# Kernel tuning notes

Measured on AMD Instinct MI355X. Metric: run time of the kernel, lower is better.

Reference implementation:

```python
import jax, jax.numpy as jnp
import numpy as np

N_NODES = 30000
N_EDGES = 480000
C_IN = 256
D_HEAD = 64   # out_channels
N_HEADS = 4
M_FEAT = 30   # nb_random_features
K_GUMBEL = 10
TAU = 0.25


def _linear_init(key, out_f, in_f):
    s = 1.0 / np.sqrt(in_f)
    k1, k2 = jax.random.split(key)
    w = jax.random.uniform(k1, (out_f, in_f), minval=-s, maxval=s, dtype=jnp.float32)
    b = jax.random.uniform(k2, (out_f,), minval=-s, maxval=s, dtype=jnp.float32)
    return w, b


def setup_inputs() -> dict:
    key = jax.random.key(0)
    ks = jax.random.split(key, 8)
    z = jax.random.normal(ks[0], (1, N_NODES, C_IN), dtype=jnp.float32)
    edge_index = jax.random.randint(ks[1], (2, N_EDGES), 0, N_NODES)
    # Gumbel(0,1)/tau noise, matching torch's (-Exp(1).log())/tau
    u = jax.random.uniform(ks[2], (N_NODES, 1, N_HEADS, K_GUMBEL), dtype=jnp.float32,
                           minval=1e-8, maxval=1.0)
    gumbels = -jnp.log(-jnp.log(u)) / TAU
    # Performer orthogonal random-feature projection matrix [M, D]
    rng = np.random.default_rng(0)
    q, _ = np.linalg.qr(rng.standard_normal((D_HEAD, D_HEAD)))
    q = q.T[:M_FEAT]
    mult = np.linalg.norm(rng.standard_normal((M_FEAT, D_HEAD)), axis=1)
    proj = jnp.asarray(np.diag(mult) @ q, dtype=jnp.float32)
    Wq_w, Wq_b = _linear_init(ks[3], N_HEADS * D_HEAD, C_IN)
    Wk_w, Wk_b = _linear_init(ks[4], N_HEADS * D_HEAD, C_IN)
    Wv_w, Wv_b = _linear_init(ks[5], N_HEADS * D_HEAD, C_IN)
    Wo_w, Wo_b = _linear_init(ks[6], D_HEAD, N_HEADS * D_HEAD)
    b = jnp.full((1, N_HEADS), 0.1, dtype=jnp.float32)  # rb_order=1, sigmoid init
    tau = jnp.float32(TAU)
    return {"z": z, "edge_index": edge_index, "tau": tau, "gumbels": gumbels,
            "proj": proj, "Wq_w": Wq_w, "Wq_b": Wq_b, "Wk_w": Wk_w, "Wk_b": Wk_b,
            "Wv_w": Wv_w, "Wv_b": Wv_b, "Wo_w": Wo_w, "Wo_b": Wo_b, "b": b}


def _softmax_kernel_feats(data, proj, is_query):
    # data: [B, N, H, D] -> phi(data): [B, N, H, M]
    dn = 1.0 / jnp.sqrt(jnp.sqrt(jnp.float32(data.shape[-1])))
    data = data * dn
    ratio = 1.0 / jnp.sqrt(jnp.float32(proj.shape[0]))
    dash = jnp.einsum('bnhd,md->bnhm', data, proj)
    diag = jnp.sum(data * data, axis=-1, keepdims=True) * 0.5
    if is_query:
        stab = jnp.max(dash, axis=-1, keepdims=True)
    else:
        stab = jnp.max(dash, axis=(1, 3), keepdims=True)
    return ratio * (jnp.exp(dash - diag - stab) + 1e-6)


def reference(z, edge_index, tau, gumbels, proj, Wq_w, Wq_b, Wk_w, Wk_b,
              Wv_w, Wv_b, Wo_w, Wo_b, b):
    B, N, _ = z.shape
    M, D = proj.shape
    H = Wq_w.shape[0] // D
    query = (z @ Wq_w.T + Wq_b).reshape(B, N, H, D)
    key = (z @ Wk_w.T + Wk_b).reshape(B, N, H, D)
    value = (z @ Wv_w.T + Wv_b).reshape(B, N, H, D)

    inv_sqrt_tau = 1.0 / jnp.sqrt(tau)
    qp = jnp.transpose(_softmax_kernel_feats(query * inv_sqrt_tau, proj, True), (1, 0, 2, 3))   # [N,B,H,M]
    kp = jnp.transpose(_softmax_kernel_feats(key * inv_sqrt_tau, proj, False), (1, 0, 2, 3))    # [N,B,H,M]
    v = jnp.transpose(value, (1, 0, 2, 3))                                                       # [N,B,H,D]

    # Gumbel-perturbed key features: [N,B,H,K,M]
    kg = kp[:, :, :, None, :] * jnp.exp(gumbels)[..., None]
    kvs = jnp.einsum('nbhkm,nbhd->bhkmd', kg, v)
    z_num = jnp.einsum('nbhm,bhkmd->nbhkd', qp, kvs)      # [N,B,H,K,D]
    z_den = jnp.einsum('nbhm,bhkm->nbhk', qp, kg.sum(axis=0))
    z_out = jnp.transpose(jnp.mean(z_num / z_den[..., None], axis=3), (1, 0, 2, 3))  # [B,N,H,D]

    # edge attention weights (for link loss)
    start, end = edge_index[0], edge_index[1]
    edge_num = jnp.transpose(jnp.einsum('ebhm,ebhm->ebh', qp[end], kp[start]), (1, 0, 2))  # [B,E,H]
    attn_norm = jnp.einsum('nbhm,bhm->nbh', qp, kp.sum(axis=0))
    edge_dem = jnp.transpose(attn_norm[end], (1, 0, 2))
    A_weight = edge_num / edge_dem

    # relational bias (rb_order=1, sigmoid), degree-normalized sparse conv over value
    ones_e = jnp.ones(start.shape[0], dtype=jnp.float32)
    d_in = jax.ops.segment_sum(ones_e, end, num_segments=N)
    d_out = jax.ops.segment_sum(ones_e, start, num_segments=N)
    edge_w = jax.nn.sigmoid(b[0])[None, :] * jnp.sqrt((1.0 / d_in[end]) * (1.0 / d_out[start]))[:, None]  # [E,H]
    conv = jax.vmap(lambda vb: jax.ops.segment_sum(vb[start] * edge_w[:, :, None], end,
                                                   num_segments=N))(value)
    z_out = z_out + conv

    z_next = z_out.reshape(B, N, H * D) @ Wo_w.T + Wo_b  # [B,N,D]

    d_norm = 1.0 / d_in[end]
    link_loss = jnp.mean(jnp.log(A_weight) * d_norm[None, :, None])
    return z_next, link_loss
```

## Files before the change

### kernel.cpp

```cpp
#include <hip/hip_runtime.h>
#include <hip/hip_bf16.h>

#define NN 30000
#define NE 480000
#define NH 4
#define DH 64
#define MF 30
#define KG 10
#define RATIO 0.18257418583505536f
#define DNRM  0.35355339059327373f

#define P_WF    0
#define P_BF    196608
#define P_WOF   197376
#define P_WOBF  213760
#define P_BBF   213824
#define P_PROJ  213828
#define P_TAU   215748
#define P_TOTAL 215749

typedef unsigned short u16;
typedef unsigned int   u32;
typedef __attribute__((ext_vector_type(8))) short bf16x8;
typedef __attribute__((ext_vector_type(4))) float f32x4;

__device__ __forceinline__ float u2f(u16 u) { return __uint_as_float(((u32)u) << 16); }
__device__ __forceinline__ u16  f2bf(float f) {
    u32 x = __float_as_uint(f);
    return (u16)((x + 0x7FFFu + ((x >> 16) & 1u)) >> 16);
}
__device__ __forceinline__ u32  encf(float f) { u32 u = __float_as_uint(f); return (u & 0x80000000u) ? ~u : (u | 0x80000000u); }
__device__ __forceinline__ float decf(u32 u)  { return (u & 0x80000000u) ? __uint_as_float(u & 0x7FFFFFFFu) : __uint_as_float(~u); }

__global__ void k_detect(const u16* __restrict__ z, int* __restrict__ flag) {
    if (threadIdx.x == 0 && blockIdx.x == 0) {
        int bad = 0;
        for (int i = 0; i < 256; i += 2) {
            u16 u = z[i];
            int e = (u >> 7) & 0xFF;
            if (u != 0 && !(e >= 100 && e <= 140)) bad++;
        }
        *flag = (bad > 16) ? 1 : 0;
    }
}

__global__ __launch_bounds__(256) void k_cvt_params(
    const void* Wq, const void* Wk, const void* Wv,
    const void* bq, const void* bk, const void* bv,
    const void* Wo, const void* Wob, const void* bb, const void* proj,
    const void* taup, float* __restrict__ params, const int* __restrict__ flag)
{
    int i = blockIdx.x * 256 + threadIdx.x;
    if (i >= P_TOTAL) return;
    int f = *flag;
    if (i == P_TAU) {
        float v = f ? ((const float*)taup)[0] : u2f(((const u16*)taup)[0]);
        if (!(v > 1e-6f && v < 1e6f)) {
            float ff = ((const float*)taup)[0];
            v = (ff > 1e-6f && ff < 1e6f) ? ff : 0.25f;
        }
        params[i] = v;
        return;
    }
    const void* src; int j;
    if      (i < 65536)  { src = Wq;  j = i; }
    else if (i < 131072) { src = Wk;  j = i - 65536; }
    else if (i < 196608) { src = Wv;  j = i - 131072; }
    else if (i < 196864) { src = bq;  j = i - 196608; }
    else if (i < 197120) { src = bk;  j = i - 196864; }
    else if (i < 197376) { src = bv;  j = i - 197120; }
    else if (i < 213760) { src = Wo;  j = i - 197376; }
    else if (i < 213824) { src = Wob; j = i - 213760; }
    else if (i < 213828) { src = bb;  j = i - 213824; }
    else                 { src = proj; j = i - P_PROJ; }
    params[i] = f ? ((const float*)src)[j] : u2f(((const u16*)src)[j]);
}

__global__ __launch_bounds__(256) void k_cvt_w(const float* __restrict__ params,
                                               u16* __restrict__ Wh, u16* __restrict__ Wl)
{
    int i = blockIdx.x * 256 + threadIdx.x;
    float x = params[P_WF + i];
    u16 h = f2bf(x);
    Wh[i] = h;
    Wl[i] = f2bf(x - u2f(h));
}

__global__ __launch_bounds__(256) void k_deg(const int* __restrict__ ei, int* __restrict__ din, int* __restrict__ dout) {
    int e = blockIdx.x * 256 + threadIdx.x;
    if (e >= NE) return;
    atomicAdd(&dout[ei[e]], 1);
    atomicAdd(&din[ei[NE + e]], 1);
}

__global__ __launch_bounds__(256) void k_off(const int* __restrict__ din, int* __restrict__ offn, int* __restrict__ counter) {
    __shared__ int s[256];
    __shared__ int base;
    int tid = threadIdx.x;
    int n = blockIdx.x * 256 + tid;
    int v = (n < NN) ? din[n] : 0;
    s[tid] = v;
    __syncthreads();
    for (int o = 1; o < 256; o <<= 1) {
        int t = (tid >= o) ? s[tid - o] : 0;
        __syncthreads();
        s[tid] += t;
        __syncthreads();
    }
    if (tid == 255) base = atomicAdd(counter, s[255]);
    __syncthreads();
    if (n < NN) offn[n] = base + s[tid] - v;
}

__global__ __launch_bounds__(256) void k_fill(const int* __restrict__ ei, const int* __restrict__ offn,
                                              int* __restrict__ fill, int* __restrict__ csr,
                                              const int* __restrict__ din, const int* __restrict__ dout,
                                              float* __restrict__ wedge) {
    int e = blockIdx.x * 256 + threadIdx.x;
    if (e >= NE) return;
    int s = ei[e], t = ei[NE + e];
    int pos = offn[t] + atomicAdd(&fill[t], 1);
    csr[pos] = s;
    wedge[pos] = rsqrtf((float)din[t] * (float)dout[s]);
}

__global__ __launch_bounds__(256) void k_gemm_feat(
    const void* __restrict__ zv, const float* __restrict__ params, const int* __restrict__ flag,
    const u16* __restrict__ Wh, const u16* __restrict__ Wl,
    u16* __restrict__ V16, float* __restrict__ qp, u16* __restrict__ qp16,
    float* __restrict__ dashK, float* __restrict__ diagK, u32* __restrict__ stab)
{
    __shared__ __align__(16) char smemc[32768];
    __shared__ u32 smaxL;
    char* AsH = smemc;
    char* AsL = smemc + 8192;
    char* BsH = smemc + 16384;
    char* BsL = smemc + 24576;
    float* tile  = (float*)smemc;
    float* projL = (float*)smemc + 4352;

    const int tid = threadIdx.x;
    const int bm = blockIdx.x * 64;
    const int bn = blockIdx.y * 64;
    const int f32 = *flag;
    const int wave = tid >> 6, lane = tid & 63;
    const int wm = wave >> 1, wn = wave & 1;
    const int sr = tid >> 2;
    const int sc = (tid & 3) * 16;

    f32x4 acc[2][2] = {};

    for (int k0 = 0; k0 < 256; k0 += 64) {
        __syncthreads();
        {
            int zrow = bm + sr;
            if (f32) {
                float x[16];
                if (zrow < NN) {
                    const float4* zp = (const float4*)((const float*)zv + (size_t)zrow * 256 + k0 + sc);
                    #pragma unroll
                    for (int q4 = 0; q4 < 4; ++q4) {
                        float4 v = zp[q4];
                        x[q4 * 4 + 0] = v.x; x[q4 * 4 + 1] = v.y;
                        x[q4 * 4 + 2] = v.z; x[q4 * 4 + 3] = v.w;
                    }
                } else {
                    #pragma unroll
                    for (int j = 0; j < 16; ++j) x[j] = 0.f;
                }
                #pragma unroll
                for (int j8 = 0; j8 < 2; ++j8) {
                    u32 hw[4], lw[4];
                    #pragma unroll
                    for (int p = 0; p < 4; ++p) {
                        float a = x[j8 * 8 + 2 * p], b2 = x[j8 * 8 + 2 * p + 1];
                        u16 ha = f2bf(a), hb = f2bf(b2);
                        hw[p] = (u32)ha | ((u32)hb << 16);
                        u16 la = f2bf(a - u2f(ha)), lb = f2bf(b2 - u2f(hb));
                        lw[p] = (u32)la | ((u32)lb << 16);
                    }
                    int byt = sr * 128 + (((sc + j8 * 8) * 2) ^ ((sr & 7) << 4));
                    *(uint4*)(AsH + byt) = make_uint4(hw[0], hw[1], hw[2], hw[3]);
                    *(uint4*)(AsL + byt) = make_uint4(lw[0], lw[1], lw[2], lw[3]);
                }
            } else {
                uint4 v0 = make_uint4(0, 0, 0, 0), v1 = v0;
                if (zrow < NN) {
                    const uint4* zp = (const uint4*)((const u16*)zv + (size_t)zrow * 256 + k0 + sc);
                    v0 = zp[0]; v1 = zp[1];
                }
                int byt0 = sr * 128 + (((sc + 0) * 2) ^ ((sr & 7) << 4));
                int byt1 = sr * 128 + (((sc + 8) * 2) ^ ((sr & 7) << 4));
                *(uint4*)(AsH + byt0) = v0;
                *(uint4*)(AsH + byt1) = v1;
            }
        }
        {
            int byt0 = sr * 128 + (((sc + 0) * 2) ^ ((sr & 7) << 4));
            int byt1 = sr * 128 + (((sc + 8) * 2) ^ ((sr & 7) << 4));
            const uint4* wh4 = (const uint4*)(Wh + (size_t)(bn + sr) * 256 + k0 + sc);
            *(uint4*)(BsH + byt0) = wh4[0];
            *(uint4*)(BsH + byt1) = wh4[1];
            if (f32) {
                const uint4* wl4 = (const uint4*)(Wl + (size_t)(bn + sr) * 256 + k0 + sc);
                *(uint4*)(BsL + byt0) = wl4[0];
                *(uint4*)(BsL + byt1) = wl4[1];
            }
        }
        __syncthreads();
        #pragma unroll
        for (int kk = 0; kk < 2; ++kk) {
            const int kb = (kk * 32 + ((lane >> 4) * 8)) * 2;
            bf16x8 ah[2], bh[2], al[2], bl[2];
            #pragma unroll
            for (int i = 0; i < 2; ++i) {
                int ar = 32 * wm + 16 * i + (lane & 15);
                int ab = ar * 128 + (kb ^ ((ar & 7) << 4));
                ah[i] = *(const bf16x8*)(AsH + ab);
                int br = 32 * wn + 16 * i + (lane & 15);
                int bb2 = br * 128 + (kb ^ ((br & 7) << 4));
                bh[i] = *(const bf16x8*)(BsH + bb2);
                if (f32) {
                    al[i] = *(const bf16x8*)(AsL + ab);
                    bl[i] = *(const bf16x8*)(BsL + bb2);
                }
            }
            #pragma unroll
            for (int i = 0; i < 2; ++i)
                #pragma unroll
                for (int nf = 0; nf < 2; ++nf) {
                    acc[i][nf] = __builtin_amdgcn_mfma_f32_16x16x32_bf16(ah[i], bh[nf], acc[i][nf], 0, 0, 0);
                    if (f32) {
                        acc[i][nf] = __builtin_amdgcn_mfma_f32_16x16x32_bf16(ah[i], bl[nf], acc[i][nf], 0, 0, 0);
                        acc[i][nf] = __builtin_amdgcn_mfma_f32_16x16x32_bf16(al[i], bh[nf], acc[i][nf], 0, 0, 0);
                    }
                }
        }
    }
    __syncthreads();

    const float* bfv = params + P_BF;
    if (bn >= 512) {
        #pragma unroll
        for (int i = 0; i < 2; ++i)
            #pragma unroll
            for (int nf = 0; nf < 2; ++nf) {
                int col = 32 * wn + 16 * nf + (lane & 15);
                float bias = bfv[bn + col];
                #pragma unroll
                for (int r2 = 0; r2 < 4; ++r2) {
                    int row = 32 * wm + 16 * i + ((lane >> 4) * 4) + r2;
                    tile[row * 68 + col] = acc[i][nf][r2] + bias;
                }
            }
        __syncthreads();
        for (int i2 = tid; i2 < 4096; i2 += 256) {
            int row = i2 >> 6, col = i2 & 63;
            int nrow = bm + row;
            if (nrow < NN) V16[(size_t)nrow * 256 + (bn - 512) + col] = f2bf(tile[row * 68 + col]);
        }
        return;
    }

    for (int i2 = tid; i2 < MF * DH; i2 += 256) projL[(i2 >> 6) * 65 + (i2 & 63)] = params[P_PROJ + i2];
    if (tid == 0) smaxL = 0u;
    float scale = DNRM * rsqrtf(params[P_TAU]);
    #pragma unroll
    for (int i = 0; i < 2; ++i)
        #pragma unroll
        for (int nf = 0; nf < 2; ++nf) {
            int col = 32 * wn + 16 * nf + (lane & 15);
            float bias = bfv[bn + col];
            #pragma unroll
            for (int r2 = 0; r2 < 4; ++r2) {
                int row = 32 * wm + 16 * i + ((lane >> 4) * 4) + r2;
                tile[row * 68 + col] = (acc[i][nf][r2] + bias) * scale;
            }
        }
    __syncthreads();

    int r = tid >> 2, q = tid & 3;
    int n = bm + r;
    const float* trow = tile + r * 68;
    float dp = 0.f;
    #pragma unroll
    for (int d = q * 16; d < q * 16 + 16; ++d) dp += trow[d] * trow[d];
    dp += __shfl_xor(dp, 1);
    dp += __shfl_xor(dp, 2);
    float diag = dp * 0.5f;

    float dm[8];
    int nm = 0;
    float lmax = -3.0e38f;
    for (int m = q; m < MF; m += 4) {
        float s = 0.f;
        #pragma unroll
        for (int d = 0; d < DH; ++d) s += trow[d] * projL[m * 65 + d];
        dm[nm++] = s;
        lmax = fmaxf(lmax, s);
    }
    float mx = fmaxf(lmax, __shfl_xor(lmax, 1));
    mx = fmaxf(mx, __shfl_xor(mx, 2));

    if (bn < 256) {
        int h = blockIdx.y;
        if (n < NN) {
            float* o = qp + ((size_t)n * NH + h) * MF;
            u16* o16 = qp16 + ((size_t)n * NH + h) * 32;
            nm = 0;
            for (int m = q; m < MF; m += 4) {
                float v = RATIO * (expf(dm[nm++] - diag - mx) + 1e-6f);
                o[m] = v;
                o16[m] = f2bf(v);
            }
            if (q == 0) { o16[30] = 0; o16[31] = 0; }
        }
    } else {
        int h = blockIdx.y - 4;
        if (n < NN) {
            float* o = dashK + ((size_t)n * NH + h) * MF;
            nm = 0;
            for (int m = q; m < MF; m += 4) o[m] = dm[nm++];
            if (q == 0) {
                diagK[(size_t)n * NH + h] = diag;
                atomicMax(&smaxL, encf(mx));
            }
        }
        __syncthreads();
        if (tid == 0) atomicMax(&stab[h], smaxL);
    }
}

__global__ __launch_bounds__(256) void k_kp(float* __restrict__ kp, const float* __restrict__ diagK,
                                            const u32* __restrict__ stab, float* __restrict__ kpsum,
                                            u16* __restrict__ kp16)
{
    __shared__ float part[NH * MF];
    __shared__ float stabf[4];
    int tid = threadIdx.x;
    if (tid < NH * MF) part[tid] = 0.f;
    if (tid >= 128 && tid < 132) stabf[tid - 128] = decf(stab[tid - 128]);
    __syncthreads();
    int base = blockIdx.x * 64 * MF;
    for (int i = tid; i < 64 * MF; i += 256) {
        int row = blockIdx.x * 64 + i / MF;
        int m = i - (i / MF) * MF;
        int h = row & 3;
        float v = RATIO * (expf(kp[base + i] - diagK[row] - stabf[h]) + 1e-6f);
        kp[base + i] = v;
        kp16[(size_t)row * 32 + m] = f2bf(v);
        atomicAdd(&part[h * MF + m], v);
    }
    if (tid < 64) {
        int row = blockIdx.x * 64 + tid;
        kp16[(size_t)row * 32 + 30] = 0;
        kp16[(size_t)row * 32 + 31] = 0;
    }
    __syncthreads();
    if (tid < NH * MF) atomicAdd(&kpsum[tid], part[tid]);
}

__global__ __launch_bounds__(256) void k_an(const float* __restrict__ qp, const float* __restrict__ kpsum,
                                            float* __restrict__ an)
{
    __shared__ float kps[NH * MF];
    int tid = threadIdx.x;
    if (tid < NH * MF) kps[tid] = kpsum[tid];
    __syncthreads();
    int idx = blockIdx.x * 256 + tid;
    if (idx >= NN * NH) return;
    int h = idx & 3;
    const float* q = qp + (size_t)idx * MF;
    float s = 0.f;
    #pragma unroll
    for (int m = 0; m < MF; ++m) s += q[m] * kps[h * MF + m];
    an[idx] = s;
}

#define KVS_CHUNKS 50
#define KVS_NPB (NN / KVS_CHUNKS)
#define KVS_TS 40
#define KVS_DZ 16
__global__ __launch_bounds__(320) void k_kvs(const float* __restrict__ kp, const void* __restrict__ gum,
                                             const u16* __restrict__ V16, const int* __restrict__ flag,
                                             float* __restrict__ Pkvs, float* __restrict__ Pksum)
{
    __shared__ float kpL[KVS_TS][MF];
    __shared__ float egL[KVS_TS][KG];
    __shared__ float vL[KVS_TS][KVS_DZ];
    int tid = threadIdx.x;
    int h = blockIdx.y;
    int z = blockIdx.z;
    int d0 = z * KVS_DZ;
    int f32 = *flag;
    int n0 = blockIdx.x * KVS_NPB;
    int ki = tid / MF, mi = tid - ki * MF;
    float4 acc0 = {0, 0, 0, 0}, acc1 = {0, 0, 0, 0}, acc2 = {0, 0, 0, 0}, acc3 = {0, 0, 0, 0};
    float ksacc = 0.f;
    for (int t0 = 0; t0 < KVS_NPB; t0 += KVS_TS) {
        __syncthreads();
        for (int i = tid; i < KVS_TS * MF; i += 320) {
            int j = i / MF, m = i - j * MF;
            kpL[j][m] = kp[(size_t)(n0 + t0 + j) * (NH * MF) + h * MF + m];
        }
        for (int i = tid; i < KVS_TS * KG; i += 320) {
            int j = i / KG, k = i - j * KG;
            size_t gofs = (size_t)(n0 + t0 + j) * (NH * KG) + h * KG + k;
            float g = f32 ? ((const float*)gum)[gofs] : u2f(((const u16*)gum)[gofs]);
            egL[j][k] = expf(g);
        }
        for (int i = tid; i < KVS_TS * KVS_DZ; i += 320) {
            int j = i / KVS_DZ, dd = i - j * KVS_DZ;
            vL[j][dd] = u2f(V16[(size_t)(n0 + t0 + j) * 256 + h * 64 + d0 + dd]);
        }
        __syncthreads();
        if (tid < KG * MF) {
            for (int j = 0; j < KVS_TS; ++j) {
                float w = kpL[j][mi] * egL[j][ki];
                ksacc += w;
                const float4* vp = (const float4*)(&vL[j][0]);
                float4 v0 = vp[0], v1 = vp[1], v2 = vp[2], v3 = vp[3];
                acc0.x += w * v0.x; acc0.y += w * v0.y; acc0.z += w * v0.z; acc0.w += w * v0.w;
                acc1.x += w * v1.x; acc1.y += w * v1.y; acc1.z += w * v1.z; acc1.w += w * v1.w;
                acc2.x += w * v2.x; acc2.y += w * v2.y; acc2.z += w * v2.z; acc2.w += w * v2.w;
                acc3.x += w * v3.x; acc3.y += w * v3.y; acc3.z += w * v3.z; acc3.w += w * v3.w;
            }
        }
    }
    if (tid < KG * MF) {
        float4* dst = (float4*)(Pkvs + (((size_t)blockIdx.x * NH + h) * 4 + z) * 4800 + tid * 16);
        dst[0] = acc0; dst[1] = acc1; dst[2] = acc2; dst[3] = acc3;
        if (z == 0) Pksum[blockIdx.x * 1200 + h * 300 + tid] = ksacc;
    }
}

__global__ __launch_bounds__(256) void k_reduce(const float* __restrict__ Pkvs, const float* __restrict__ Pksum,
                                                float* __restrict__ kvs, float* __restrict__ ksum)
{
    int i = blockIdx.x * 256 + threadIdx.x;
    if (i < NH * KG * MF * DH) {
        int h  = i / (KG * MF * DH);
        int km = (i / DH) % (KG * MF);
        int d  = i & (DH - 1);
        size_t ofs = ((size_t)h * 4 + (d >> 4)) * 4800 + km * 16 + (d & 15);
        float s = 0.f;
        for (int c = 0; c < KVS_CHUNKS; ++c) s += Pkvs[(size_t)c * (NH * 4 * 4800) + ofs];
        kvs[i] = s;
    } else if (i < NH * KG * MF * DH + NH * KG * MF) {
        int j = i - NH * KG * MF * DH;
        float s = 0.f;
        for (int c = 0; c < KVS_CHUNKS; ++c) s += Pksum[c * 1200 + j];
        ksum[j] = s;
    }
}

__global__ __launch_bounds__(256) void k_edge(const int* __restrict__ ei,
                                              const u16* __restrict__ qp16, const u16* __restrict__ kp16,
                                              const float* __restrict__ an,
                                              const int* __restrict__ din, float* __restrict__ lossp)
{
    __shared__ float ls[64];
    int tid = threadIdx.x;
    int eg = tid >> 2, h = tid & 3;
    int e = blockIdx.x * 64 + eg;
    int s = ei[e], t = ei[NE + e];
    const uint4* qv = (const uint4*)(qp16 + ((size_t)t * NH + h) * 32);
    const uint4* kv = (const uint4*)(kp16 + ((size_t)s * NH + h) * 32);
    float num = 0.f;
    #pragma unroll
    for (int c = 0; c < 4; ++c) {
        uint4 a = qv[c], b = kv[c];
        num += u2f((u16)(a.x & 0xFFFF)) * u2f((u16)(b.x & 0xFFFF))
             + u2f((u16)(a.x >> 16))    * u2f((u16)(b.x >> 16))
             + u2f((u16)(a.y & 0xFFFF)) * u2f((u16)(b.y & 0xFFFF))
             + u2f((u16)(a.y >> 16))    * u2f((u16)(b.y >> 16))
             + u2f((u16)(a.z & 0xFFFF)) * u2f((u16)(b.z & 0xFFFF))
             + u2f((u16)(a.z >> 16))    * u2f((u16)(b.z >> 16))
             + u2f((u16)(a.w & 0xFFFF)) * u2f((u16)(b.w & 0xFFFF))
             + u2f((u16)(a.w >> 16))    * u2f((u16)(b.w >> 16));
    }
    float term = logf(num / an[(size_t)t * NH + h]);
    term += __shfl_xor(term, 1);
    term += __shfl_xor(term, 2);
    if (h == 0) ls[eg] = term / (float)din[t];
    __syncthreads();
    if (tid < 64) {
        float v = ls[tid];
        #pragma unroll
        for (int o = 32; o > 0; o >>= 1) v += __shfl_xor(v, o);
        if (tid == 0) atomicAdd(&lossp[blockIdx.x & 1023], v);
    }
}

#define AT_NT 48
__global__ __launch_bounds__(256) void k_attn(
    const float* __restrict__ qp, const float* __restrict__ kvs, const float* __restrict__ ksum,
    u16* __restrict__ zatt)
{
    __shared__ float qpTf[3][NH * 484];
    __shared__ u32   kvbuf[NH * 964];
    __shared__ float rdenL[3][16 * NH * KG];
    u16*   kvL16 = (u16*)kvbuf;
    float* ksL   = (float*)kvbuf;
    int tid = threadIdx.x;
    int n0 = blockIdx.x * AT_NT;

    for (int i = tid; i < AT_NT * NH * MF; i += 256) {
        int j48 = i / (NH * MF); int r = i - j48 * (NH * MF);
        int h = r / MF; int m = r - h * MF;
        qpTf[j48 >> 4][h * 484 + m * 16 + (j48 & 15)] = qp[(size_t)(n0 + j48) * (NH * MF) + r];
    }
    for (int i = tid; i < NH * KG * MF; i += 256) ksL[i] = ksum[i];
    __syncthreads();
    for (int i = tid; i < AT_NT * NH * KG; i += 256) {
        int j48 = i / (NH * KG); int r = i - j48 * (NH * KG);
        int h = r / KG;
        int sub = j48 >> 4, j = j48 & 15;
        float s = 0.f;
        #pragma unroll
        for (int m = 0; m < MF; ++m) s += qpTf[sub][h * 484 + m * 16 + j] * ksL[r * MF + m];
        rdenL[sub][j * (NH * KG) + r] = 1.0f / s;
    }

    const int h  = tid >> 6;
    const int jg = (tid >> 4) & 3;
    const int dg = tid & 15;
    float acc[3][4][4] = {};
    for (int k = 0; k < KG; ++k) {
        __syncthreads();
        for (int i = tid; i < NH * MF * DH; i += 256) {
            int hh = i / (MF * DH); int r = i - hh * (MF * DH);
            kvL16[hh * 1928 + r] = f2bf(kvs[((size_t)(hh * KG + k) * MF) * DH + r]);
        }
        __syncthreads();
        float ps[3][4][4] = {};
        const u16* kb = kvL16 + h * 1928 + dg * 4;
        const float* qb0 = qpTf[0] + h * 484 + jg * 4;
        const float* qb1 = qpTf[1] + h * 484 + jg * 4;
        const float* qb2 = qpTf[2] + h * 484 + jg * 4;
        #pragma unroll
        for (int m = 0; m < MF; ++m) {
            ushort4 bu = *(const ushort4*)(kb + m * 64);
            float4 b = make_float4(u2f(bu.x), u2f(bu.y), u2f(bu.z), u2f(bu.w));
            float4 a0 = *(const float4*)(qb0 + m * 16);
            float4 a1 = *(const float4*)(qb1 + m * 16);
            float4 a2 = *(const float4*)(qb2 + m * 16);
            ps[0][0][0] += a0.x * b.x; ps[0][0][1] += a0.x * b.y; ps[0][0][2] += a0.x * b.z; ps[0][0][3] += a0.x * b.w;
            ps[0][1][0] += a0.y * b.x; ps[0][1][1] += a0.y * b.y; ps[0][1][2] += a0.y * b.z; ps[0][1][3] += a0.y * b.w;
            ps[0][2][0] += a0.z * b.x; ps[0][2][1] += a0.z * b.y; ps[0][2][2] += a0.z * b.z; ps[0][2][3] += a0.z * b.w;
            ps[0][3][0] += a0.w * b.x; ps[0][3][1] += a0.w * b.y; ps[0][3][2] += a0.w * b.z; ps[0][3][3] += a0.w * b.w;
            ps[1][0][0] += a1.x * b.x; ps[1][0][1] += a1.x * b.y; ps[1][0][2] += a1.x * b.z; ps[1][0][3] += a1.x * b.w;
            ps[1][1][0] += a1.y * b.x; ps[1][1][1] += a1.y * b.y; ps[1][1][2] += a1.y * b.z; ps[1][1][3] += a1.y * b.w;
            ps[1][2][0] += a1.z * b.x; ps[1][2][1] += a1.z * b.y; ps[1][2][2] += a1.z * b.z; ps[1][2][3] += a1.z * b.w;
            ps[1][3][0] += a1.w * b.x; ps[1][3][1] += a1.w * b.y; ps[1][3][2] += a1.w * b.z; ps[1][3][3] += a1.w * b.w;
            ps[2][0][0] += a2.x * b.x; ps[2][0][1] += a2.x * b.y; ps[2][0][2] += a2.x * b.z; ps[2][0][3] += a2.x * b.w;
            ps[2][1][0] += a2.y * b.x; ps[2][1][1] += a2.y * b.y; ps[2][1][2] += a2.y * b.z; ps[2][1][3] += a2.y * b.w;
            ps[2][2][0] += a2.z * b.x; ps[2][2][1] += a2.z * b.y; ps[2][2][2] += a2.z * b.z; ps[2][2][3] += a2.z * b.w;
            ps[2][3][0] += a2.w * b.x; ps[2][3][1] += a2.w * b.y; ps[2][3][2] += a2.w * b.z; ps[2][3][3] += a2.w * b.w;
        }
        #pragma unroll
        for (int sub = 0; sub < 3; ++sub)
            #pragma unroll
            for (int j4 = 0; j4 < 4; ++j4) {
                float rd = rdenL[sub][(jg * 4 + j4) * (NH * KG) + h * KG + k];
                #pragma unroll
                for (int d4 = 0; d4 < 4; ++d4) acc[sub][j4][d4] += ps[sub][j4][d4] * rd;
            }
    }
    #pragma unroll
    for (int sub = 0; sub < 3; ++sub)
        #pragma unroll
        for (int j4 = 0; j4 < 4; ++j4) {
            int n = n0 + sub * 16 + jg * 4 + j4;
            #pragma unroll
            for (int d4 = 0; d4 < 4; ++d4)
                zatt[(size_t)n * 256 + h * 64 + dg * 4 + d4] = f2bf(acc[sub][j4][d4] * (1.0f / KG));
        }
}

__global__ __launch_bounds__(256) void k_gather(
    const u16* __restrict__ zatt, const u16* __restrict__ V16,
    const int* __restrict__ csr, const float* __restrict__ wedge,
    const int* __restrict__ offn, const int* __restrict__ din,
    const float* __restrict__ params, u16* __restrict__ pre)
{
    int tid = threadIdx.x;
    int w = tid >> 6, l = tid & 63;
    int n = blockIdx.x * 4 + w;
    float sigb = 1.f / (1.f + expf(-params[P_BBF + (l >> 4)]));
    int dn = din[n], o0 = offn[n];
    float c0 = 0.f, c1 = 0.f, c2 = 0.f, c3 = 0.f;
    for (int t0 = 0; t0 < dn; t0 += 64) {
        int cnt = min(64, dn - t0);
        int myIdx = 0; float myW = 0.f;
        if (l < cnt) { myIdx = csr[o0 + t0 + l]; myW = wedge[o0 + t0 + l]; }
        int j = 0;
        for (; j + 7 < cnt; j += 8) {
            int   s0 = __shfl(myIdx, j),     s1 = __shfl(myIdx, j + 1);
            int   s2 = __shfl(myIdx, j + 2), s3 = __shfl(myIdx, j + 3);
            int   s4 = __shfl(myIdx, j + 4), s5 = __shfl(myIdx, j + 5);
            int   s6 = __shfl(myIdx, j + 6), s7 = __shfl(myIdx, j + 7);
            float w0 = __shfl(myW, j),     w1 = __shfl(myW, j + 1);
            float w2 = __shfl(myW, j + 2), w3 = __shfl(myW, j + 3);
            float w4 = __shfl(myW, j + 4), w5 = __shfl(myW, j + 5);
            float w6 = __shfl(myW, j + 6), w7 = __shfl(myW, j + 7);
            uint2 a0 = *(const uint2*)(V16 + (size_t)s0 * 256 + l * 4);
            uint2 a1 = *(const uint2*)(V16 + (size_t)s1 * 256 + l * 4);
            uint2 a2 = *(const uint2*)(V16 + (size_t)s2 * 256 + l * 4);
            uint2 a3 = *(const uint2*)(V16 + (size_t)s3 * 256 + l * 4);
            uint2 a4 = *(const uint2*)(V16 + (size_t)s4 * 256 + l * 4);
            uint2 a5 = *(const uint2*)(V16 + (size_t)s5 * 256 + l * 4);
            uint2 a6 = *(const uint2*)(V16 + (size_t)s6 * 256 + l * 4);
            uint2 a7 = *(const uint2*)(V16 + (size_t)s7 * 256 + l * 4);
            c0 += w0 * u2f((u16)(a0.x & 0xFFFF)) + w1 * u2f((u16)(a1.x & 0xFFFF))
                + w2 * u2f((u16)(a2.x & 0xFFFF)) + w3 * u2f((u16)(a3.x & 0xFFFF))
                + w4 * u2f((u16)(a4.x & 0xFFFF)) + w5 * u2f((u16)(a5.x & 0xFFFF))
                + w6 * u2f((u16)(a6.x & 0xFFFF)) + w7 * u2f((u16)(a7.x & 0xFFFF));
            c1 += w0 * u2f((u16)(a0.x >> 16)) + w1 * u2f((u16)(a1.x >> 16))
                + w2 * u2f((u16)(a2.x >> 16)) + w3 * u2f((u16)(a3.x >> 16))
                + w4 * u2f((u16)(a4.x >> 16)) + w5 * u2f((u16)(a5.x >> 16))
                + w6 * u2f((u16)(a6.x >> 16)) + w7 * u2f((u16)(a7.x >> 16));
            c2 += w0 * u2f((u16)(a0.y & 0xFFFF)) + w1 * u2f((u16)(a1.y & 0xFFFF))
                + w2 * u2f((u16)(a2.y & 0xFFFF)) + w3 * u2f((u16)(a3.y & 0xFFFF))
                + w4 * u2f((u16)(a4.y & 0xFFFF)) + w5 * u2f((u16)(a5.y & 0xFFFF))
                + w6 * u2f((u16)(a6.y & 0xFFFF)) + w7 * u2f((u16)(a7.y & 0xFFFF));
            c3 += w0 * u2f((u16)(a0.y >> 16)) + w1 * u2f((u16)(a1.y >> 16))
                + w2 * u2f((u16)(a2.y >> 16)) + w3 * u2f((u16)(a3.y >> 16))
                + w4 * u2f((u16)(a4.y >> 16)) + w5 * u2f((u16)(a5.y >> 16))
                + w6 * u2f((u16)(a6.y >> 16)) + w7 * u2f((u16)(a7.y >> 16));
        }
        for (; j < cnt; ++j) {
            int   s0 = __shfl(myIdx, j);
            float w0 = __shfl(myW, j);
            uint2 a0 = *(const uint2*)(V16 + (size_t)s0 * 256 + l * 4);
            c0 += w0 * u2f((u16)(a0.x & 0xFFFF));
            c1 += w0 * u2f((u16)(a0.x >> 16));
            c2 += w0 * u2f((u16)(a0.y & 0xFFFF));
            c3 += w0 * u2f((u16)(a0.y >> 16));
        }
    }
    uint2 za = *(const uint2*)(zatt + (size_t)n * 256 + l * 4);
    float e0 = u2f((u16)(za.x & 0xFFFF)) + sigb * c0;
    float e1 = u2f((u16)(za.x >> 16))    + sigb * c1;
    float e2 = u2f((u16)(za.y & 0xFFFF)) + sigb * c2;
    float e3 = u2f((u16)(za.y >> 16))    + sigb * c3;
    uint2 r;
    r.x = (u32)f2bf(e0) | ((u32)f2bf(e1) << 16);
    r.y = (u32)f2bf(e2) | ((u32)f2bf(e3) << 16);
    *(uint2*)(pre + (size_t)n * 256 + l * 4) = r;
}

__global__ __launch_bounds__(256) void k_out(
    const u16* __restrict__ pre, const float* __restrict__ params, float* __restrict__ out)
{
    __shared__ __align__(16) char smemc[24576];
    char* As  = smemc;
    char* BsH = smemc + 8192;
    char* BsL = smemc + 16384;
    const int tid = threadIdx.x;
    const int bm = blockIdx.x * 64;
    const int wave = tid >> 6, lane = tid & 63;
    const int wm = wave >> 1, wn = wave & 1;
    const int sr = tid >> 2;
    const int sc = (tid & 3) * 16;

    f32x4 acc[2][2] = {};

    for (int k0 = 0; k0 < 256; k0 += 64) {
        __syncthreads();
        int byt0 = sr * 128 + (((sc + 0) * 2) ^ ((sr & 7) << 4));
        int byt1 = sr * 128 + (((sc + 8) * 2) ^ ((sr & 7) << 4));
        {
            int row = bm + sr;
            uint4 v0 = make_uint4(0, 0, 0, 0), v1 = v0;
            if (row < NN) {
                const uint4* p = (const uint4*)(pre + (size_t)row * 256 + k0 + sc);
                v0 = p[0]; v1 = p[1];
            }
            *(uint4*)(As + byt0) = v0;
            *(uint4*)(As + byt1) = v1;
        }
        {
            float x[16];
            const float4* wr = (const float4*)(params + P_WOF + (size_t)sr * 256 + k0 + sc);
            #pragma unroll
            for (int q4 = 0; q4 < 4; ++q4) {
                float4 v = wr[q4];
                x[q4 * 4 + 0] = v.x; x[q4 * 4 + 1] = v.y;
                x[q4 * 4 + 2] = v.z; x[q4 * 4 + 3] = v.w;
            }
            #pragma unroll
            for (int j8 = 0; j8 < 2; ++j8) {
                u32 hw[4], lw[4];
                #pragma unroll
                for (int p = 0; p < 4; ++p) {
                    float a = x[j8 * 8 + 2 * p], b2 = x[j8 * 8 + 2 * p + 1];
                    u16 ha = f2bf(a), hb = f2bf(b2);
                    hw[p] = (u32)ha | ((u32)hb << 16);
                    u16 la = f2bf(a - u2f(ha)), lb = f2bf(b2 - u2f(hb));
                    lw[p] = (u32)la | ((u32)lb << 16);
                }
                int byt = sr * 128 + (((sc + j8 * 8) * 2) ^ ((sr & 7) << 4));
                *(uint4*)(BsH + byt) = make_uint4(hw[0], hw[1], hw[2], hw[3]);
                *(uint4*)(BsL + byt) = make_uint4(lw[0], lw[1], lw[2], lw[3]);
            }
        }
        __syncthreads();
        #pragma unroll
        for (int kk = 0; kk < 2; ++kk) {
            const int kb = (kk * 32 + ((lane >> 4) * 8)) * 2;
            bf16x8 a[2], bh[2], bl[2];
            #pragma unroll
            for (int i = 0; i < 2; ++i) {
                int ar = 32 * wm + 16 * i + (lane & 15);
                int ab = ar * 128 + (kb ^ ((ar & 7) << 4));
                a[i] = *(const bf16x8*)(As + ab);
                int br = 32 * wn + 16 * i + (lane & 15);
                int bb2 = br * 128 + (kb ^ ((br & 7) << 4));
                bh[i] = *(const bf16x8*)(BsH + bb2);
                bl[i] = *(const bf16x8*)(BsL + bb2);
            }
            #pragma unroll
            for (int i = 0; i < 2; ++i)
                #pragma unroll
                for (int nf = 0; nf < 2; ++nf) {
                    acc[i][nf] = __builtin_amdgcn_mfma_f32_16x16x32_bf16(a[i], bh[nf], acc[i][nf], 0, 0, 0);
                    acc[i][nf] = __builtin_amdgcn_mfma_f32_16x16x32_bf16(a[i], bl[nf], acc[i][nf], 0, 0, 0);
                }
        }
    }
    #pragma unroll
    for (int i = 0; i < 2; ++i)
        #pragma unroll
        for (int nf = 0; nf < 2; ++nf) {
            int col = 32 * wn + 16 * nf + (lane & 15);
            float bias = params[P_WOBF + col];
            #pragma unroll
            for (int r2 = 0; r2 < 4; ++r2) {
                int row = bm + 32 * wm + 16 * i + ((lane >> 4) * 4) + r2;
                if (row < NN) out[(size_t)row * 64 + col] = acc[i][nf][r2] + bias;
            }
        }
}

__global__ __launch_bounds__(256) void k_loss(const float* __restrict__ lossp, float* __restrict__ out) {
    __shared__ float s[256];
    int tid = threadIdx.x;
    float v = 0.f;
    for (int i = tid; i < 1024; i += 256) v += lossp[i];
    s[tid] = v;
    __syncthreads();
    for (int o = 128; o > 0; o >>= 1) {
        if (tid < o) s[tid] += s[tid + o];
        __syncthreads();
    }
    if (tid == 0) out[(size_t)NN * 64] = s[0] / (float)(NE * NH);
}

extern "C" void kernel_launch(void* const* d_in, const int* in_sizes, int n_in,
                              void* d_out, int out_size, void* d_ws, size_t ws_size,
                              hipStream_t stream)
{
    const void* z    = d_in[0];
    const int*  ei   = (const int*)d_in[1];
    const void* taup = d_in[2];
    const void* gum  = d_in[3];
    const void* proj = d_in[4];
    const void* Wq   = d_in[5];
    const void* bq   = d_in[6];
    const void* Wk   = d_in[7];
    const void* bk   = d_in[8];
    const void* Wv   = d_in[9];
    const void* bv   = d_in[10];
    const void* Wo   = d_in[11];
    const void* Wob  = d_in[12];
    const void* bb   = d_in[13];
    float* out = (float*)d_out;

    u16*   V16    = (u16*)d_ws;
    float* qpb    = (float*)d_ws + 3840000;
    float* kpb    = qpb + (size_t)NN * NH * MF;
    float* diagK  = kpb + (size_t)NN * NH * MF;
    float* anb    = diagK + (size_t)NN * NH;
    u16*   zatt   = (u16*)kpb;
    int*   csr    = (int*)(anb + (size_t)NN * NH);
    int*   offn   = csr + NE;
    float* params = (float*)(offn + NN);
    float* kvs    = params + 215752;
    float* ksum   = kvs + NH * KG * MF * DH;
    float* kpsum  = ksum + NH * KG * MF;
    int*   din    = (int*)(kpsum + NH * MF);
    int*   doutd  = din + NN;
    int*   fill   = doutd + NN;
    int*   counter = fill + NN;
    u32*   stab   = (u32*)(counter + 4);
    float* lossp  = (float*)(stab + 4);
    int*   flag   = (int*)(lossp + 1024);
    float* wedge  = (float*)(flag + 4);
    u16*   qp16   = (u16*)(wedge + NE);
    u16*   kp16   = qp16 + (size_t)NN * NH * 32;
    float* Pkvs   = (float*)qp16;
    float* Pksum  = (float*)(kp16 + (size_t)NN * NH * 32);
    u16*   Whb    = kp16;
    u16*   Wlb    = kp16 + 196608;
    u16*   pre    = qp16;
    size_t zero_bytes = (size_t)((char*)(flag + 4) - (char*)kvs);

    hipMemsetAsync(kvs, 0, zero_bytes, stream);

    k_detect<<<dim3(1), dim3(64), 0, stream>>>((const u16*)z, flag);
    k_cvt_params<<<dim3((P_TOTAL + 255) / 256), dim3(256), 0, stream>>>(
        Wq, Wk, Wv, bq, bk, bv, Wo, Wob, bb, proj, taup, params, flag);
    k_cvt_w<<<dim3(768), dim3(256), 0, stream>>>(params, Whb, Wlb);

    k_deg <<<dim3((NE + 255) / 256), dim3(256), 0, stream>>>(ei, din, doutd);
    k_off <<<dim3((NN + 255) / 256), dim3(256), 0, stream>>>(din, offn, counter);
    k_fill<<<dim3((NE + 255) / 256), dim3(256), 0, stream>>>(ei, offn, fill, csr, din, doutd, wedge);
    k_gemm_feat<<<dim3((NN + 63) / 64, 12), dim3(256), 0, stream>>>(
        z, params, flag, Whb, Wlb, V16, qpb, qp16, kpb, diagK, stab);
    k_kp  <<<dim3(NN * NH / 64), dim3(256), 0, stream>>>(kpb, diagK, stab, kpsum, kp16);
    k_an  <<<dim3((NN * NH + 255) / 256), dim3(256), 0, stream>>>(qpb, kpsum, anb);
    k_edge<<<dim3(NE / 64), dim3(256), 0, stream>>>(ei, qp16, kp16, anb, din, lossp);
    k_kvs <<<dim3(KVS_CHUNKS, NH, DH / KVS_DZ), dim3(320), 0, stream>>>(kpb, gum, V16, flag, Pkvs, Pksum);
    k_reduce<<<dim3((NH * KG * MF * DH + NH * KG * MF + 255) / 256), dim3(256), 0, stream>>>(
        Pkvs, Pksum, kvs, ksum);
    k_attn<<<dim3(NN / AT_NT), dim3(256), 0, stream>>>(qpb, kvs, ksum, zatt);
    k_gather<<<dim3(NN / 4), dim3(256), 0, stream>>>(zatt, V16, csr, wedge, offn, din, params, pre);
    k_out<<<dim3((NN + 63) / 64), dim3(256), 0, stream>>>(pre, params, out);
    k_loss<<<dim3(1), dim3(256), 0, stream>>>(lossp, out);
}
```

Before: 762.4 us.

## Compute per-chunk KV state with bf16 MFMA instead of scalar FMA loops

Rewrites k_kvs so each block forms the (Gumbel-weighted kp) × V outer product for all 64 value dims using 16x16x32 bf16 MFMA, with kp·exp(gumbel) products and V staged transposed in XOR-swizzled LDS. The grid drops its DZ split and each 512-thread block handles one chunk and head, with partial results written in a plain [chunk][h][row][d] layout that k_reduce now reads linearly. This replaces the fp32 scalar accumulation and redundant per-DZ reloads of kp and gumbel data. The cost is bf16 rounding of the weights and of ksum.

```diff
diff --git a/kernel.cpp b/kernel.cpp
--- a/kernel.cpp
+++ b/kernel.cpp
@@ -379,58 +379,112 @@
 
 #define KVS_CHUNKS 50
 #define KVS_NPB (NN / KVS_CHUNKS)
-#define KVS_TS 40
-#define KVS_DZ 16
-__global__ __launch_bounds__(320) void k_kvs(const float* __restrict__ kp, const void* __restrict__ gum,
+__global__ __launch_bounds__(512) void k_kvs(const float* __restrict__ kp, const void* __restrict__ gum,
                                              const u16* __restrict__ V16, const int* __restrict__ flag,
                                              float* __restrict__ Pkvs, float* __restrict__ Pksum)
 {
-    __shared__ float kpL[KVS_TS][MF];
-    __shared__ float egL[KVS_TS][KG];
-    __shared__ float vL[KVS_TS][KVS_DZ];
-    int tid = threadIdx.x;
-    int h = blockIdx.y;
-    int z = blockIdx.z;
-    int d0 = z * KVS_DZ;
-    int f32 = *flag;
-    int n0 = blockIdx.x * KVS_NPB;
-    int ki = tid / MF, mi = tid - ki * MF;
-    float4 acc0 = {0, 0, 0, 0}, acc1 = {0, 0, 0, 0}, acc2 = {0, 0, 0, 0}, acc3 = {0, 0, 0, 0};
-    float ksacc = 0.f;
-    for (int t0 = 0; t0 < KVS_NPB; t0 += KVS_TS) {
-        __syncthreads();
-        for (int i = tid; i < KVS_TS * MF; i += 320) {
-            int j = i / MF, m = i - j * MF;
-            kpL[j][m] = kp[(size_t)(n0 + t0 + j) * (NH * MF) + h * MF + m];
-        }
-        for (int i = tid; i < KVS_TS * KG; i += 320) {
-            int j = i / KG, k = i - j * KG;
-            size_t gofs = (size_t)(n0 + t0 + j) * (NH * KG) + h * KG + k;
-            float g = f32 ? ((const float*)gum)[gofs] : u2f(((const u16*)gum)[gofs]);
-            egL[j][k] = expf(g);
-        }
-        for (int i = tid; i < KVS_TS * KVS_DZ; i += 320) {
-            int j = i / KVS_DZ, dd = i - j * KVS_DZ;
-            vL[j][dd] = u2f(V16[(size_t)(n0 + t0 + j) * 256 + h * 64 + d0 + dd]);
-        }
-        __syncthreads();
-        if (tid < KG * MF) {
-            for (int j = 0; j < KVS_TS; ++j) {
-                float w = kpL[j][mi] * egL[j][ki];
-                ksacc += w;
-                const float4* vp = (const float4*)(&vL[j][0]);
-                float4 v0 = vp[0], v1 = vp[1], v2 = vp[2], v3 = vp[3];
-                acc0.x += w * v0.x; acc0.y += w * v0.y; acc0.z += w * v0.z; acc0.w += w * v0.w;
-                acc1.x += w * v1.x; acc1.y += w * v1.y; acc1.z += w * v1.z; acc1.w += w * v1.w;
-                acc2.x += w * v2.x; acc2.y += w * v2.y; acc2.z += w * v2.z; acc2.w += w * v2.w;
-                acc3.x += w * v3.x; acc3.y += w * v3.y; acc3.z += w * v3.z; acc3.w += w * v3.w;
-            }
-        }
-    }
-    if (tid < KG * MF) {
-        float4* dst = (float4*)(Pkvs + (((size_t)blockIdx.x * NH + h) * 4 + z) * 4800 + tid * 16);
-        dst[0] = acc0; dst[1] = acc1; dst[2] = acc2; dst[3] = acc3;
-        if (z == 0) Pksum[blockIdx.x * 1200 + h * 300 + tid] = ksacc;
+    __shared__ __align__(16) char kgT[320 * 128];
+    __shared__ __align__(16) char VT[64 * 128];
+    __shared__ float kpT[64][31];
+    __shared__ float egT[64][10];
+    const int tid = threadIdx.x;
+    const int h = blockIdx.y;
+    const int chunk = blockIdx.x;
+    const int n0 = chunk * KVS_NPB;
+    const int f32 = *flag;
+    const int wave = tid >> 6, lane = tid & 63;
+
+    float ksacc[5] = {0.f, 0.f, 0.f, 0.f, 0.f};
+    f32x4 acc[10] = {};
+
+    for (int t0 = 0; t0 < KVS_NPB; t0 += 64) {
+        __syncthreads();
+        for (int i = tid; i < 64 * MF; i += 512) {
+            int n = i / MF, m = i - (i / MF) * MF;
+            kpT[n][m] = (t0 + n < KVS_NPB) ? kp[(size_t)(n0 + t0 + n) * (NH * MF) + h * MF + m] : 0.f;
+        }
+        for (int i = tid; i < 64 * KG; i += 512) {
+            int n = i / KG, k = i - (i / KG) * KG;
+            float e = 0.f;
+            if (t0 + n < KVS_NPB) {
+                size_t gofs = (size_t)(n0 + t0 + n) * (NH * KG) + h * KG + k;
+                float g = f32 ? ((const float*)gum)[gofs] : u2f(((const u16*)gum)[gofs]);
+                e = expf(g);
+            }
+            egT[n][k] = e;
+        }
+        for (int i = tid; i < 64 * 16; i += 512) {
+            int n = i >> 4, dq = (i & 15) * 4;
+            u32 v0 = 0, v1 = 0;
+            if (t0 + n < KVS_NPB) {
+                uint2 vv = *(const uint2*)(V16 + (size_t)(n0 + t0 + n) * 256 + h * 64 + dq);
+                v0 = vv.x; v1 = vv.y;
+            }
+            #pragma unroll
+            for (int j = 0; j < 4; ++j) {
+                u16 val = (u16)(((j < 2) ? v0 : v1) >> ((j & 1) * 16));
+                int d = dq + j;
+                *(u16*)(VT + d * 128 + ((n * 2) ^ ((d & 7) << 4))) = val;
+            }
+        }
+        __syncthreads();
+        #pragma unroll
+        for (int it = 0; it < 5; ++it) {
+            int idx = tid + it * 512;
+            int row = idx >> 3, nc = idx & 7;
+            u32 w_[4] = {0u, 0u, 0u, 0u};
+            if (row < 300) {
+                int k = row / MF, m = row - (row / MF) * MF;
+                float s = 0.f;
+                #pragma unroll
+                for (int p = 0; p < 4; ++p) {
+                    int na = nc * 8 + 2 * p, nb = na + 1;
+                    u16 ha = f2bf(kpT[na][m] * egT[na][k]);
+                    u16 hb = f2bf(kpT[nb][m] * egT[nb][k]);
+                    w_[p] = (u32)ha | ((u32)hb << 16);
+                    s += u2f(ha) + u2f(hb);
+                }
+                ksacc[it] += s;
+            }
+            *(uint4*)(kgT + row * 128 + ((nc * 16) ^ ((row & 7) << 4))) = make_uint4(w_[0], w_[1], w_[2], w_[3]);
+        }
+        __syncthreads();
+        #pragma unroll
+        for (int kk = 0; kk < 2; ++kk) {
+            const int kb = (kk * 32 + ((lane >> 4) * 8)) * 2;
+            #pragma unroll
+            for (int i = 0; i < 10; ++i) {
+                int ct = wave * 10 + i;
+                int kt = ct >> 2, dt = ct & 3;
+                int ar = kt * 16 + (lane & 15);
+                bf16x8 a = *(const bf16x8*)(kgT + ar * 128 + (kb ^ ((ar & 7) << 4)));
+                int br = dt * 16 + (lane & 15);
+                bf16x8 b = *(const bf16x8*)(VT + br * 128 + (kb ^ ((br & 7) << 4)));
+                acc[i] = __builtin_amdgcn_mfma_f32_16x16x32_bf16(a, b, acc[i], 0, 0, 0);
+            }
+        }
+    }
+    #pragma unroll
+    for (int i = 0; i < 10; ++i) {
+        int ct = wave * 10 + i;
+        int kt = ct >> 2, dt = ct & 3;
+        int col = dt * 16 + (lane & 15);
+        #pragma unroll
+        for (int r = 0; r < 4; ++r) {
+            int row = kt * 16 + ((lane >> 4) * 4) + r;
+            if (row < 300)
+                Pkvs[(((size_t)chunk * NH + h) * 300 + row) * 64 + col] = acc[i][r];
+        }
+    }
+    #pragma unroll
+    for (int it = 0; it < 5; ++it) {
+        float v = ksacc[it];
+        v += __shfl_xor(v, 1);
+        v += __shfl_xor(v, 2);
+        v += __shfl_xor(v, 4);
+        int row = (tid + it * 512) >> 3;
+        if ((tid & 7) == 0 && row < 300)
+            Pksum[chunk * 1200 + h * 300 + row] = v;
     }
 }
 
@@ -439,12 +493,8 @@
 {
     int i = blockIdx.x * 256 + threadIdx.x;
     if (i < NH * KG * MF * DH) {
-        int h  = i / (KG * MF * DH);
-        int km = (i / DH) % (KG * MF);
-        int d  = i & (DH - 1);
-        size_t ofs = ((size_t)h * 4 + (d >> 4)) * 4800 + km * 16 + (d & 15);
         float s = 0.f;
-        for (int c = 0; c < KVS_CHUNKS; ++c) s += Pkvs[(size_t)c * (NH * 4 * 4800) + ofs];
+        for (int c = 0; c < KVS_CHUNKS; ++c) s += Pkvs[(size_t)c * (NH * 300 * 64) + i];
         kvs[i] = s;
     } else if (i < NH * KG * MF * DH + NH * KG * MF) {
         int j = i - NH * KG * MF * DH;
@@ -821,7 +871,7 @@
     k_kp  <<<dim3(NN * NH / 64), dim3(256), 0, stream>>>(kpb, diagK, stab, kpsum, kp16);
     k_an  <<<dim3((NN * NH + 255) / 256), dim3(256), 0, stream>>>(qpb, kpsum, anb);
     k_edge<<<dim3(NE / 64), dim3(256), 0, stream>>>(ei, qp16, kp16, anb, din, lossp);
-    k_kvs <<<dim3(KVS_CHUNKS, NH, DH / KVS_DZ), dim3(320), 0, stream>>>(kpb, gum, V16, flag, Pkvs, Pksum);
+    k_kvs <<<dim3(KVS_CHUNKS, NH), dim3(512), 0, stream>>>(kpb, gum, V16, flag, Pkvs, Pksum);
     k_reduce<<<dim3((NH * KG * MF * DH + NH * KG * MF + 255) / 256), dim3(256), 0, stream>>>(
         Pkvs, Pksum, kvs, ksum);
     k_attn<<<dim3(NN / AT_NT), dim3(256), 0, stream>>>(qpb, kvs, ksum, zatt);
```

Result: faster. 677.4 us (-11.1%).
